# Kernel tuning notes

Hardware: AMD Instinct MI355X
Metric: run time of the kernel (lower is better)

Reference implementation:

```python
import jax, jax.numpy as jnp
import numpy as np

HEADS = 8
DIM_HEAD = 64
DIM = 512
HIDDEN = HEADS * DIM_HEAD  # 512


def setup_inputs() -> dict:
    key = jax.random.key(0)
    k1, k2, k3, k4 = jax.random.split(key, 4)
    b, m, n = 4, 8, 512
    x = jax.random.normal(k1, (b, m, n, DIM), dtype=jnp.float32)
    pos_bias = jax.random.normal(k2, (HEADS, n, 16, 16), dtype=jnp.float32)
    # torch nn.Linear(dim, 3*hidden) weight is [3*hidden, dim]; we store the
    # transposed matmul form [dim, 3*hidden] for y = x @ W.
    w_qkv = jax.random.normal(k3, (DIM, 3 * HIDDEN), dtype=jnp.float32) * (DIM ** -0.5)
    w_out = jax.random.normal(k4, (HIDDEN, DIM), dtype=jnp.float32) * (HIDDEN ** -0.5)
    return {"x": x, "pos_bias": pos_bias, "w_qkv": w_qkv, "w_out": w_out}


def reference(x, pos_bias, w_qkv, w_out):
    b, m, n, _ = x.shape
    h, d = HEADS, DIM_HEAD
    scale = d ** -0.5
    qkv = jnp.einsum('bmnc,ce->bmne', x, w_qkv)  # [b,m,n,3*hidden]
    q, k, v = jnp.split(qkv, 3, axis=-1)
    # 'b m n (h d) -> (b m) h n d'
    def to_heads(t):
        return t.reshape(b * m, n, h, d).transpose(0, 2, 1, 3)
    q, k, v = to_heads(q), to_heads(k), to_heads(v)
    q = q * scale
    sim = jnp.einsum('bhid,bhjd->bhij', q, k)  # [(b*m), h, n, n]
    # pos_bias [h, n, p, q] -> mean over last two dims -> [h, n] -> broadcast [1,h,n,1]
    pb = pos_bias.mean(axis=(-2, -1))[None, :, :, None]
    sim = sim + pb
    sim = sim - jax.lax.stop_gradient(jnp.max(sim, axis=-1, keepdims=True))
    attn = jax.nn.softmax(sim, axis=-1)
    out = jnp.einsum('bhij,bhjd->bhid', attn, v)  # [(b*m), h, n, d]
    # '(b m) h n d -> b m n (h d)'
    out = out.transpose(0, 2, 1, 3).reshape(b, m, n, h * d)
    return jnp.einsum('bmne,ec->bmnc', out, w_out)
```

## Files before the change

kernel.cpp:

```cpp
#include <hip/hip_runtime.h>
#include <stdint.h>


typedef __attribute__((ext_vector_type(8))) short bf16x8;
typedef __attribute__((ext_vector_type(4))) float f32x4;
typedef __attribute__((ext_vector_type(4))) unsigned short us4;
typedef __attribute__((ext_vector_type(4))) float float4v;

__device__ __forceinline__ unsigned short f2b(float f) {
  union { float f; uint32_t u; } x; x.f = f;
  uint32_t r = x.u + 0x7fffu + ((x.u >> 16) & 1u);
  return (unsigned short)(r >> 16);
}

__device__ __forceinline__ uint32_t cvtpk(float lo, float hi) {
  uint32_t r;
  asm("v_cvt_pk_bf16_f32 %0, %1, %2" : "=v"(r) : "v"(lo), "v"(hi));
  return r;
}

__device__ __forceinline__ f32x4 mfma16(bf16x8 a, bf16x8 b, f32x4 c) {
  return __builtin_amdgcn_mfma_f32_16x16x32_bf16(a, b, c, 0, 0, 0);
}

__device__ __forceinline__ void gload_lds16(const unsigned short* g, unsigned short* l) {
  __builtin_amdgcn_global_load_lds(
      (const __attribute__((address_space(1))) unsigned int*)g,
      (__attribute__((address_space(3))) unsigned int*)l, 16, 0, 0);
}

__global__ __launch_bounds__(256) void cast_x_kernel(
    const float* __restrict__ src, unsigned short* __restrict__ dst) {
  size_t i = ((size_t)blockIdx.x * 256 + threadIdx.x) * 4;
  float4v v = *(const float4v*)(src + i);
  us4 o;
#pragma unroll
  for (int j = 0; j < 4; ++j) o[j] = f2b(v[j]);
  *(us4*)(dst + i) = o;
}

__global__ __launch_bounds__(256) void transpose_cast_kernel(
    const float* __restrict__ src, unsigned short* __restrict__ dst, int R, int C) {
  __shared__ float tile[64][65];
  const int tc0 = blockIdx.x * 64;
  const int tr0 = blockIdx.y * 64;
#pragma unroll
  for (int k2 = 0; k2 < 16; ++k2) {
    int idx = threadIdx.x + k2 * 256;
    int r = idx >> 6, c = idx & 63;
    tile[r][c] = src[(size_t)(tr0 + r) * C + tc0 + c];
  }
  __syncthreads();
#pragma unroll
  for (int k2 = 0; k2 < 16; ++k2) {
    int idx = threadIdx.x + k2 * 256;
    int c = idx >> 6, r = idx & 63;
    dst[(size_t)(tc0 + c) * R + tr0 + r] = f2b(tile[r][c]);
  }
}

__device__ __forceinline__ void gemm_core(
    const unsigned short* __restrict__ A, const unsigned short* __restrict__ Bt,
    int K, int r0, int c0, unsigned short* As, unsigned short* Bs,
    f32x4 (&acc)[4][4]) {
  const int tid = threadIdx.x;
  const int lane = tid & 63;
  const int wave = tid >> 6;
  const int wr = (wave >> 1) * 64;
  const int wc = (wave & 1) * 64;
  const int l15 = lane & 15;
  const int g = lane >> 4;
  const int lsw = l15 & 7;

#pragma unroll
  for (int m = 0; m < 4; ++m)
#pragma unroll
    for (int n = 0; n < 4; ++n) acc[m][n] = (f32x4){0.f, 0.f, 0.f, 0.f};

  auto stage = [&](int kt, int b) {
#pragma unroll
    for (int i = 0; i < 4; ++i) {
      int chunk = tid + i * 256;
      int row = chunk >> 3;
      int csw = (chunk & 7) ^ (row & 7);
      gload_lds16(A + (size_t)(r0 + row) * K + kt + csw * 8,
                  As + b * 8192 + chunk * 8);
      gload_lds16(Bt + (size_t)(c0 + row) * K + kt + csw * 8,
                  Bs + b * 8192 + chunk * 8);
    }
  };

  stage(0, 0);
  asm volatile("s_waitcnt vmcnt(0)" ::: "memory");
  __builtin_amdgcn_s_barrier();

  const int NT = K >> 6;
  int cur = 0;
  for (int t = 0; t < NT; ++t) {
    if (t + 1 < NT) stage((t + 1) << 6, cur ^ 1);
    const unsigned short* as = As + cur * 8192;
    const unsigned short* bs = Bs + cur * 8192;
#pragma unroll
    for (int ks = 0; ks < 2; ++ks) {
      bf16x8 af[4], bfr[4];
      const int j = g + ks * 4;
      const int cj = (j ^ lsw) * 8;
#pragma unroll
      for (int m = 0; m < 4; ++m)
        af[m] = *(const bf16x8*)(as + (wr + m * 16 + l15) * 64 + cj);
#pragma unroll
      for (int n = 0; n < 4; ++n)
        bfr[n] = *(const bf16x8*)(bs + (wc + n * 16 + l15) * 64 + cj);
      __builtin_amdgcn_s_setprio(1);
#pragma unroll
      for (int m = 0; m < 4; ++m)
#pragma unroll
        for (int n = 0; n < 4; ++n) acc[m][n] = mfma16(af[m], bfr[n], acc[m][n]);
      __builtin_amdgcn_s_setprio(0);
    }
    if (t + 1 < NT) {
      asm volatile("s_waitcnt vmcnt(0)" ::: "memory");
      __builtin_amdgcn_s_barrier();
      cur ^= 1;
    }
  }
  __syncthreads();
}

__global__ __launch_bounds__(256) void gemm_qkv_kernel(
    const unsigned short* __restrict__ xb, const unsigned short* __restrict__ wqbT,
    unsigned short* __restrict__ qb, unsigned short* __restrict__ kb,
    unsigned short* __restrict__ vtb) {
  __shared__ unsigned short smem[32768];
  f32x4 acc[4][4];
  const int r0 = blockIdx.x * 128;
  const int c0 = blockIdx.y * 128;
  gemm_core(xb, wqbT, 512, r0, c0, smem, smem + 16384, acc);

  const int tid = threadIdx.x, lane = tid & 63, wave = tid >> 6;
  const int wr = (wave >> 1) * 64, wc = (wave & 1) * 64;
  const int l15 = lane & 15, g = lane >> 4;
  const int part = c0 >> 9;
  const float scl = (part == 0) ? 0.125f : 1.0f;

  if (part < 2) {
#pragma unroll
    for (int m = 0; m < 4; ++m) {
      int rbase = wr + m * 16 + 4 * g;
#pragma unroll
      for (int n = 0; n < 4; ++n) {
        int c = wc + n * 16 + l15;
        int c2 = c >> 3, ci = c & 7;
#pragma unroll
        for (int rr = 0; rr < 4; ++rr) {
          int r = rbase + rr;
          smem[r * 128 + ((c2 ^ (r & 15)) << 3) + ci] = f2b(acc[m][n][rr] * scl);
        }
      }
    }
    __syncthreads();
    unsigned short* dstb = (part == 0) ? qb : kb;
#pragma unroll
    for (int it = 0; it < 8; ++it) {
      int idx = tid + it * 256;
      int r = idx >> 4, c2 = idx & 15;
      bf16x8 v = *(const bf16x8*)(smem + r * 128 + ((c2 ^ (r & 15)) << 3));
      int e = c0 + c2 * 8;
      int rem = e & 511, h = rem >> 6, d = rem & 63;
      int ig = r0 + r;
      int bh = (ig >> 9) * 8 + h, i = ig & 511;
      *(bf16x8*)(dstb + ((size_t)bh * 512 + i) * 64 + d) = v;
    }
  } else {
#pragma unroll
    for (int m = 0; m < 4; ++m) {
      int rbase = wr + m * 16 + 4 * g;
      int r2 = rbase >> 3, rhalf = rbase & 7;
#pragma unroll
      for (int n = 0; n < 4; ++n) {
        int c = wc + n * 16 + l15;
        us4 v;
#pragma unroll
        for (int rr = 0; rr < 4; ++rr) v[rr] = f2b(acc[m][n][rr]);
        *(us4*)(smem + c * 128 + ((r2 ^ (c & 15)) << 3) + rhalf) = v;
      }
    }
    __syncthreads();
#pragma unroll
    for (int it = 0; it < 8; ++it) {
      int idx = tid + it * 256;
      int c = idx >> 4, r8 = idx & 15;
      bf16x8 v = *(const bf16x8*)(smem + c * 128 + ((r8 ^ (c & 15)) << 3));
      int e = c0 + c;
      int rem = e & 511, h = rem >> 6, d = rem & 63;
      int ig0 = r0 + r8 * 8;
      int bh = (ig0 >> 9) * 8 + h, i = ig0 & 511;
      *(bf16x8*)(vtb + ((size_t)bh * 64 + d) * 512 + i) = v;
    }
  }
}

__global__ __launch_bounds__(256) void gemm_out_kernel(
    const unsigned short* __restrict__ ao, const unsigned short* __restrict__ wobT,
    float* __restrict__ out) {
  __shared__ unsigned short smem[32768];
  f32x4 acc[4][4];
  const int r0 = blockIdx.x * 128;
  const int c0 = blockIdx.y * 128;
  gemm_core(ao, wobT, 512, r0, c0, smem, smem + 16384, acc);

  const int tid = threadIdx.x, lane = tid & 63, wave = tid >> 6;
  const int wr = (wave >> 1) * 64, wc = (wave & 1) * 64;
  const int l15 = lane & 15, g = lane >> 4;
#pragma unroll
  for (int m = 0; m < 4; ++m) {
    int i0g = r0 + wr + m * 16 + 4 * g;
#pragma unroll
    for (int n = 0; n < 4; ++n) {
      int e = c0 + wc + n * 16 + l15;
#pragma unroll
      for (int rr = 0; rr < 4; ++rr)
        out[(size_t)(i0g + rr) * 512 + e] = acc[m][n][rr];
    }
  }
}

__global__ __launch_bounds__(512, 4) void attn_kernel(
    const unsigned short* __restrict__ qb, const unsigned short* __restrict__ kb,
    const unsigned short* __restrict__ vtb, unsigned short* __restrict__ ao) {
  __shared__ unsigned short kbuf[2][8192];
  __shared__ unsigned short vbuf[2][8192];
  __shared__ unsigned short Ps[8][16][40];
  const int bh = blockIdx.x;
  const int qt = blockIdx.y;
  const int tid = threadIdx.x, lane = tid & 63, wave = tid >> 6;
  const int l15 = lane & 15, g = lane >> 4;
  const int qrow0 = qt * 128 + wave * 16;

  const unsigned short* Q = qb + ((size_t)bh * 512 + qrow0) * 64;
  const unsigned short* Kp = kb + (size_t)bh * 512 * 64;
  const unsigned short* Vt = vtb + (size_t)bh * 64 * 512;

  bf16x8 qf0 = *(const bf16x8*)(Q + l15 * 64 + g * 8);
  bf16x8 qf1 = *(const bf16x8*)(Q + l15 * 64 + 32 + g * 8);

  const int krow = tid >> 3;
  const int kck = (tid & 7) ^ (krow & 7);
  const int vrow = tid >> 4;
  const int vck = (tid & 15) ^ (vrow & 15);

  auto stage = [&](int t, int b) {
    const unsigned short* ks = Kp + ((size_t)t * 128 + krow) * 64 + kck * 8;
    gload_lds16(ks, kbuf[b] + tid * 8);
    gload_lds16(ks + 64 * 64, kbuf[b] + tid * 8 + 4096);
    const unsigned short* vs = Vt + (size_t)vrow * 512 + t * 128 + vck * 8;
    gload_lds16(vs, vbuf[b] + tid * 8);
    gload_lds16(vs + 32 * 512, vbuf[b] + tid * 8 + 4096);
  };

  f32x4 oacc[4];
#pragma unroll
  for (int m = 0; m < 4; ++m) oacc[m] = (f32x4){0.f, 0.f, 0.f, 0.f};
  float srow[4] = {0.f, 0.f, 0.f, 0.f};

  stage(0, 0);
  asm volatile("s_waitcnt vmcnt(0)" ::: "memory");
  __builtin_amdgcn_s_barrier();

  int cur = 0;
#pragma unroll
  for (int t = 0; t < 4; ++t) {
    if (t < 3) stage(t + 1, cur ^ 1);

    const unsigned short* kb_ = kbuf[cur];
    f32x4 s[8];
    const int c0i = g ^ (l15 & 7);
    __builtin_amdgcn_s_setprio(1);
#pragma unroll
    for (int tt = 0; tt < 8; ++tt) {
      int row = tt * 16 + l15;
      bf16x8 b0 = *(const bf16x8*)(kb_ + (row * 8 + c0i) * 8);
      bf16x8 b1 = *(const bf16x8*)(kb_ + (row * 8 + (c0i ^ 4)) * 8);
      f32x4 c = (f32x4){0.f, 0.f, 0.f, 0.f};
      c = mfma16(qf0, b0, c);
      s[tt] = mfma16(qf1, b1, c);
    }
    __builtin_amdgcn_s_setprio(0);

#pragma unroll
    for (int tt = 0; tt < 8; ++tt)
#pragma unroll
      for (int rr = 0; rr < 4; ++rr) {
        float e = __expf(s[tt][rr]);
        s[tt][rr] = e;
        srow[rr] += e;
      }

    const unsigned short* vb_ = vbuf[cur];
#pragma unroll
    for (int cc = 0; cc < 4; ++cc) {
#pragma unroll
      for (int rr = 0; rr < 4; ++rr) {
        uint32_t pk = cvtpk(s[cc * 2][rr], s[cc * 2 + 1][rr]);
        Ps[wave][4 * g + rr][l15] = (unsigned short)pk;
        Ps[wave][4 * g + rr][16 + l15] = (unsigned short)(pk >> 16);
      }
      asm volatile("s_waitcnt lgkmcnt(0)" ::: "memory");
      bf16x8 pf = *(const bf16x8*)(&Ps[wave][l15][g * 8]);
      __builtin_amdgcn_s_setprio(1);
#pragma unroll
      for (int m = 0; m < 4; ++m) {
        int vr = m * 16 + l15;
        bf16x8 vf = *(const bf16x8*)(vb_ + (vr * 16 + ((cc * 4 + g) ^ l15)) * 8);
        oacc[m] = mfma16(vf, pf, oacc[m]);
      }
      __builtin_amdgcn_s_setprio(0);
    }

    if (t < 3) {
      asm volatile("s_waitcnt vmcnt(0)" ::: "memory");
      __builtin_amdgcn_s_barrier();
      cur ^= 1;
    }
  }

#pragma unroll
  for (int rr = 0; rr < 4; ++rr)
#pragma unroll
    for (int o = 1; o < 16; o <<= 1) srow[rr] += __shfl_xor(srow[rr], o);
  int srcl = (l15 >> 2) * 16;
  float t0 = __shfl(srow[0], srcl), t1 = __shfl(srow[1], srcl);
  float t2 = __shfl(srow[2], srcl), t3 = __shfl(srow[3], srcl);
  int rq = l15 & 3;
  float sq = rq == 0 ? t0 : rq == 1 ? t1 : rq == 2 ? t2 : t3;
  float invq = 1.0f / sq;

  const int hh = bh & 7, bm = bh >> 3;
  unsigned short* aorow = ao + ((size_t)bm * 512 + qrow0 + l15) * 512 + hh * 64;
#pragma unroll
  for (int m = 0; m < 4; ++m) {
    union { us4 u; uint32_t w[2]; } uv;
    uv.w[0] = cvtpk(oacc[m][0] * invq, oacc[m][1] * invq);
    uv.w[1] = cvtpk(oacc[m][2] * invq, oacc[m][3] * invq);
    *(us4*)(aorow + m * 16 + 4 * g) = uv.u;
  }
}

extern "C" void kernel_launch(void* const* d_in, const int* in_sizes, int n_in,
                              void* d_out, int out_size, void* d_ws, size_t ws_size,
                              hipStream_t stream) {
  const float* x = (const float*)d_in[0];
  const float* w_qkv = (const float*)d_in[2];
  const float* w_out = (const float*)d_in[3];
  float* out = (float*)d_out;

  char* ws = (char*)d_ws;
  const size_t SZ_XB = 16384ull * 512 * 2;
  const size_t SZ_WQ = 1536ull * 512 * 2;
  const size_t SZ_WO = 512ull * 512 * 2;
  const size_t SZ_HB = 256ull * 512 * 64 * 2;
  unsigned short* xb = (unsigned short*)(ws);
  unsigned short* wqbT = (unsigned short*)(ws + SZ_XB);
  unsigned short* wobT = (unsigned short*)(ws + SZ_XB + SZ_WQ);
  unsigned short* qb = (unsigned short*)(ws + SZ_XB + SZ_WQ + SZ_WO);
  unsigned short* kb = (unsigned short*)(ws + SZ_XB + SZ_WQ + SZ_WO + SZ_HB);
  unsigned short* vtb = (unsigned short*)(ws + SZ_XB + SZ_WQ + SZ_WO + 2 * SZ_HB);
  unsigned short* ao = (unsigned short*)(ws + SZ_XB + SZ_WQ + SZ_WO + 3 * SZ_HB);

  cast_x_kernel<<<8192, 256, 0, stream>>>(x, xb);
  transpose_cast_kernel<<<dim3(1536 / 64, 512 / 64), 256, 0, stream>>>(w_qkv, wqbT, 512, 1536);
  transpose_cast_kernel<<<dim3(512 / 64, 512 / 64), 256, 0, stream>>>(w_out, wobT, 512, 512);
  gemm_qkv_kernel<<<dim3(128, 12), 256, 0, stream>>>(xb, wqbT, qb, kb, vtb);
  attn_kernel<<<dim3(256, 4), 512, 0, stream>>>(qb, kb, vtb, ao);
  gemm_out_kernel<<<dim3(128, 4), 256, 0, stream>>>(ao, wobT, out);
}
```

Baseline: 94.03 us.

## Use 256x128 GEMM tiles with 8 waves and triple-buffered LDS pipeline

Both projection GEMMs now use 512-thread blocks covering 256x128 output tiles, so each B tile is shared by twice as many rows. The K loop is fully unrolled over a fixed K=512 and uses a three-stage LDS ring with partial vmcnt waits, keeping two loads in flight while the current tile is computed. This aims to hide global load latency and cut the barrier stall after each K step. In exchange, it uses much more LDS per block (one block per CU), halves the grid size, and hardcodes K=512.

After: 99.41 us. 5.7% more time.

```diff
diff --git a/kernel.cpp b/kernel.cpp
--- a/kernel.cpp
+++ b/kernel.cpp
@@ -61,7 +61,7 @@
 
 __device__ __forceinline__ void gemm_core(
     const unsigned short* __restrict__ A, const unsigned short* __restrict__ Bt,
-    int K, int r0, int c0, unsigned short* As, unsigned short* Bs,
+    int r0, int c0, unsigned short* As, unsigned short* Bs,
     f32x4 (&acc)[4][4]) {
   const int tid = threadIdx.x;
   const int lane = tid & 63;
@@ -80,31 +80,37 @@
   auto stage = [&](int kt, int b) {
 #pragma unroll
     for (int i = 0; i < 4; ++i) {
-      int chunk = tid + i * 256;
+      int chunk = tid + i * 512;
       int row = chunk >> 3;
       int csw = (chunk & 7) ^ (row & 7);
-      gload_lds16(A + (size_t)(r0 + row) * K + kt + csw * 8,
-                  As + b * 8192 + chunk * 8);
-      gload_lds16(Bt + (size_t)(c0 + row) * K + kt + csw * 8,
+      gload_lds16(A + (size_t)(r0 + row) * 512 + kt + csw * 8,
+                  As + b * 16384 + chunk * 8);
+    }
+#pragma unroll
+    for (int i = 0; i < 2; ++i) {
+      int chunk = tid + i * 512;
+      int row = chunk >> 3;
+      int csw = (chunk & 7) ^ (row & 7);
+      gload_lds16(Bt + (size_t)(c0 + row) * 512 + kt + csw * 8,
                   Bs + b * 8192 + chunk * 8);
     }
   };
 
   stage(0, 0);
-  asm volatile("s_waitcnt vmcnt(0)" ::: "memory");
-  __builtin_amdgcn_s_barrier();
-
-  const int NT = K >> 6;
-  int cur = 0;
-  for (int t = 0; t < NT; ++t) {
-    if (t + 1 < NT) stage((t + 1) << 6, cur ^ 1);
-    const unsigned short* as = As + cur * 8192;
-    const unsigned short* bs = Bs + cur * 8192;
+  stage(64, 1);
+
+#pragma unroll
+  for (int t = 0; t < 8; ++t) {
+    if (t < 7) asm volatile("s_waitcnt vmcnt(6)" ::: "memory");
+    else       asm volatile("s_waitcnt vmcnt(0)" ::: "memory");
+    __builtin_amdgcn_s_barrier();
+    if (t < 6) stage((t + 2) * 64, (t + 2) % 3);
+    const unsigned short* as = As + (t % 3) * 16384;
+    const unsigned short* bs = Bs + (t % 3) * 8192;
 #pragma unroll
     for (int ks = 0; ks < 2; ++ks) {
       bf16x8 af[4], bfr[4];
-      const int j = g + ks * 4;
-      const int cj = (j ^ lsw) * 8;
+      const int cj = ((g + ks * 4) ^ lsw) * 8;
 #pragma unroll
       for (int m = 0; m < 4; ++m)
         af[m] = *(const bf16x8*)(as + (wr + m * 16 + l15) * 64 + cj);
@@ -118,24 +124,20 @@
         for (int n = 0; n < 4; ++n) acc[m][n] = mfma16(af[m], bfr[n], acc[m][n]);
       __builtin_amdgcn_s_setprio(0);
     }
-    if (t + 1 < NT) {
-      asm volatile("s_waitcnt vmcnt(0)" ::: "memory");
-      __builtin_amdgcn_s_barrier();
-      cur ^= 1;
-    }
   }
   __syncthreads();
 }
 
-__global__ __launch_bounds__(256) void gemm_qkv_kernel(
+__global__ __launch_bounds__(512, 1) void gemm_qkv_kernel(
     const unsigned short* __restrict__ xb, const unsigned short* __restrict__ wqbT,
     unsigned short* __restrict__ qb, unsigned short* __restrict__ kb,
     unsigned short* __restrict__ vtb) {
-  __shared__ unsigned short smem[32768];
+  __shared__ unsigned short As[49152];
+  __shared__ unsigned short Bs[24576];
   f32x4 acc[4][4];
-  const int r0 = blockIdx.x * 128;
+  const int r0 = blockIdx.x * 256;
   const int c0 = blockIdx.y * 128;
-  gemm_core(xb, wqbT, 512, r0, c0, smem, smem + 16384, acc);
+  gemm_core(xb, wqbT, r0, c0, As, Bs, acc);
 
   const int tid = threadIdx.x, lane = tid & 63, wave = tid >> 6;
   const int wr = (wave >> 1) * 64, wc = (wave & 1) * 64;
@@ -154,7 +156,7 @@
 #pragma unroll
         for (int rr = 0; rr < 4; ++rr) {
           int r = rbase + rr;
-          smem[r * 128 + ((c2 ^ (r & 15)) << 3) + ci] = f2b(acc[m][n][rr] * scl);
+          As[r * 128 + ((c2 ^ (r & 15)) << 3) + ci] = f2b(acc[m][n][rr] * scl);
         }
       }
     }
@@ -162,9 +164,9 @@
     unsigned short* dstb = (part == 0) ? qb : kb;
 #pragma unroll
     for (int it = 0; it < 8; ++it) {
-      int idx = tid + it * 256;
+      int idx = tid + it * 512;
       int r = idx >> 4, c2 = idx & 15;
-      bf16x8 v = *(const bf16x8*)(smem + r * 128 + ((c2 ^ (r & 15)) << 3));
+      bf16x8 v = *(const bf16x8*)(As + r * 128 + ((c2 ^ (r & 15)) << 3));
       int e = c0 + c2 * 8;
       int rem = e & 511, h = rem >> 6, d = rem & 63;
       int ig = r0 + r;
@@ -182,15 +184,15 @@
         us4 v;
 #pragma unroll
         for (int rr = 0; rr < 4; ++rr) v[rr] = f2b(acc[m][n][rr]);
-        *(us4*)(smem + c * 128 + ((r2 ^ (c & 15)) << 3) + rhalf) = v;
+        *(us4*)(As + c * 256 + ((r2 ^ (c & 31)) << 3) + rhalf) = v;
       }
     }
     __syncthreads();
 #pragma unroll
     for (int it = 0; it < 8; ++it) {
-      int idx = tid + it * 256;
-      int c = idx >> 4, r8 = idx & 15;
-      bf16x8 v = *(const bf16x8*)(smem + c * 128 + ((r8 ^ (c & 15)) << 3));
+      int idx = tid + it * 512;
+      int c = idx >> 5, r8 = idx & 31;
+      bf16x8 v = *(const bf16x8*)(As + c * 256 + ((r8 ^ (c & 31)) << 3));
       int e = c0 + c;
       int rem = e & 511, h = rem >> 6, d = rem & 63;
       int ig0 = r0 + r8 * 8;
@@ -200,14 +202,15 @@
   }
 }
 
-__global__ __launch_bounds__(256) void gemm_out_kernel(
+__global__ __launch_bounds__(512, 1) void gemm_out_kernel(
     const unsigned short* __restrict__ ao, const unsigned short* __restrict__ wobT,
     float* __restrict__ out) {
-  __shared__ unsigned short smem[32768];
+  __shared__ unsigned short As[49152];
+  __shared__ unsigned short Bs[24576];
   f32x4 acc[4][4];
-  const int r0 = blockIdx.x * 128;
+  const int r0 = blockIdx.x * 256;
   const int c0 = blockIdx.y * 128;
-  gemm_core(ao, wobT, 512, r0, c0, smem, smem + 16384, acc);
+  gemm_core(ao, wobT, r0, c0, As, Bs, acc);
 
   const int tid = threadIdx.x, lane = tid & 63, wave = tid >> 6;
   const int wr = (wave >> 1) * 64, wc = (wave & 1) * 64;
@@ -370,7 +373,7 @@
   cast_x_kernel<<<8192, 256, 0, stream>>>(x, xb);
   transpose_cast_kernel<<<dim3(1536 / 64, 512 / 64), 256, 0, stream>>>(w_qkv, wqbT, 512, 1536);
   transpose_cast_kernel<<<dim3(512 / 64, 512 / 64), 256, 0, stream>>>(w_out, wobT, 512, 512);
-  gemm_qkv_kernel<<<dim3(128, 12), 256, 0, stream>>>(xb, wqbT, qb, kb, vtb);
+  gemm_qkv_kernel<<<dim3(64, 12), 512, 0, stream>>>(xb, wqbT, qb, kb, vtb);
   attn_kernel<<<dim3(256, 4), 512, 0, stream>>>(qb, kb, vtb, ao);
-  gemm_out_kernel<<<dim3(128, 4), 256, 0, stream>>>(ao, wobT, out);
-}
+  gemm_out_kernel<<<dim3(64, 4), 512, 0, stream>>>(ao, wobT, out);
+}
```

## Fuse x fp32-to-bf16 cast into QKV GEMM and merge weight prep kernels

Applied to the files above, without the earlier changes.

The QKV GEMM now reads fp32 x directly through registers, converts it to bf16 with packed cvt, and writes the swizzled A tile to LDS. This removes the separate cast kernel and its 16 MB bf16 round trip. The two weight transpose-cast launches are merged into a single prep kernel, cutting launch count. In exchange, each QKV block re-reads fp32 x across its 12 column tiles (12x the fp32 traffic, mostly served from cache), uses register-staged A loads instead of direct-to-LDS loads, and adds register pressure under launch_bounds(256,2).

Result: slower. 99.91 us (+6.3%).

```diff
diff --git a/kernel.cpp b/kernel.cpp
--- a/kernel.cpp
+++ b/kernel.cpp
@@ -6,6 +6,7 @@
 typedef __attribute__((ext_vector_type(4))) float f32x4;
 typedef __attribute__((ext_vector_type(4))) unsigned short us4;
 typedef __attribute__((ext_vector_type(4))) float float4v;
+typedef __attribute__((ext_vector_type(2))) unsigned int ui2;
 
 __device__ __forceinline__ unsigned short f2b(float f) {
   union { float f; uint32_t u; } x; x.f = f;
@@ -29,21 +30,21 @@
       (__attribute__((address_space(3))) unsigned int*)l, 16, 0, 0);
 }
 
-__global__ __launch_bounds__(256) void cast_x_kernel(
-    const float* __restrict__ src, unsigned short* __restrict__ dst) {
-  size_t i = ((size_t)blockIdx.x * 256 + threadIdx.x) * 4;
-  float4v v = *(const float4v*)(src + i);
-  us4 o;
-#pragma unroll
-  for (int j = 0; j < 4; ++j) o[j] = f2b(v[j]);
-  *(us4*)(dst + i) = o;
-}
-
-__global__ __launch_bounds__(256) void transpose_cast_kernel(
-    const float* __restrict__ src, unsigned short* __restrict__ dst, int R, int C) {
+__global__ __launch_bounds__(256) void prep_kernel(
+    const float* __restrict__ wq, unsigned short* __restrict__ wqbT,
+    const float* __restrict__ wo, unsigned short* __restrict__ wobT) {
   __shared__ float tile[64][65];
-  const int tc0 = blockIdx.x * 64;
-  const int tr0 = blockIdx.y * 64;
+  const int bid = blockIdx.x;
+  const float* src;
+  unsigned short* dst;
+  int R, C, bx, by;
+  if (bid < 192) {
+    src = wq; dst = wqbT; R = 512; C = 1536; bx = bid % 24; by = bid / 24;
+  } else {
+    int q = bid - 192;
+    src = wo; dst = wobT; R = 512; C = 512; bx = q % 8; by = q / 8;
+  }
+  const int tc0 = bx * 64, tr0 = by * 64;
 #pragma unroll
   for (int k2 = 0; k2 < 16; ++k2) {
     int idx = threadIdx.x + k2 * 256;
@@ -59,52 +60,74 @@
   }
 }
 
-__device__ __forceinline__ void gemm_core(
-    const unsigned short* __restrict__ A, const unsigned short* __restrict__ Bt,
-    int K, int r0, int c0, unsigned short* As, unsigned short* Bs,
-    f32x4 (&acc)[4][4]) {
+__global__ __launch_bounds__(256, 2) void gemm_qkv_kernel(
+    const float* __restrict__ x, const unsigned short* __restrict__ wqbT,
+    unsigned short* __restrict__ qb, unsigned short* __restrict__ kb,
+    unsigned short* __restrict__ vtb) {
+  __shared__ unsigned short As[16384];
+  __shared__ unsigned short Bs[16384];
   const int tid = threadIdx.x;
-  const int lane = tid & 63;
-  const int wave = tid >> 6;
-  const int wr = (wave >> 1) * 64;
-  const int wc = (wave & 1) * 64;
-  const int l15 = lane & 15;
-  const int g = lane >> 4;
-  const int lsw = l15 & 7;
-
+  const int lane = tid & 63, wave = tid >> 6;
+  const int wr = (wave >> 1) * 64, wc = (wave & 1) * 64;
+  const int l15 = lane & 15, g = lane >> 4, lsw = l15 & 7;
+  const int r0 = blockIdx.x * 128;
+  const int c0 = blockIdx.y * 128;
+
+  f32x4 acc[4][4];
 #pragma unroll
   for (int m = 0; m < 4; ++m)
 #pragma unroll
     for (int n = 0; n < 4; ++n) acc[m][n] = (f32x4){0.f, 0.f, 0.f, 0.f};
 
-  auto stage = [&](int kt, int b) {
+  const int afc = tid & 15;
+  const int arow0 = tid >> 4;
+  float4v ar[8];
+  auto loadA = [&](int kt) {
+#pragma unroll
+    for (int i = 0; i < 8; ++i)
+      ar[i] = *(const float4v*)(x + (size_t)(r0 + arow0 + i * 16) * 512 + kt + afc * 4);
+  };
+  const int ac2 = afc >> 1, ah = afc & 1;
+  auto writeA = [&](int b) {
+#pragma unroll
+    for (int i = 0; i < 8; ++i) {
+      int row = arow0 + i * 16;
+      uint32_t w0 = cvtpk(ar[i][0], ar[i][1]);
+      uint32_t w1 = cvtpk(ar[i][2], ar[i][3]);
+      int cs = ac2 ^ (row & 7);
+      *(ui2*)(As + b * 8192 + row * 64 + cs * 8 + ah * 4) = (ui2){w0, w1};
+    }
+  };
+  auto stageB = [&](int kt, int b) {
 #pragma unroll
     for (int i = 0; i < 4; ++i) {
       int chunk = tid + i * 256;
       int row = chunk >> 3;
       int csw = (chunk & 7) ^ (row & 7);
-      gload_lds16(A + (size_t)(r0 + row) * K + kt + csw * 8,
-                  As + b * 8192 + chunk * 8);
-      gload_lds16(Bt + (size_t)(c0 + row) * K + kt + csw * 8,
+      gload_lds16(wqbT + (size_t)(c0 + row) * 512 + kt + csw * 8,
                   Bs + b * 8192 + chunk * 8);
     }
   };
 
-  stage(0, 0);
+  loadA(0);
+  stageB(0, 0);
   asm volatile("s_waitcnt vmcnt(0)" ::: "memory");
-  __builtin_amdgcn_s_barrier();
-
-  const int NT = K >> 6;
+  writeA(0);
+  __syncthreads();
+
   int cur = 0;
-  for (int t = 0; t < NT; ++t) {
-    if (t + 1 < NT) stage((t + 1) << 6, cur ^ 1);
+#pragma unroll
+  for (int t = 0; t < 8; ++t) {
+    if (t < 7) {
+      loadA((t + 1) * 64);
+      stageB((t + 1) * 64, cur ^ 1);
+    }
     const unsigned short* as = As + cur * 8192;
     const unsigned short* bs = Bs + cur * 8192;
 #pragma unroll
     for (int ks = 0; ks < 2; ++ks) {
       bf16x8 af[4], bfr[4];
-      const int j = g + ks * 4;
-      const int cj = (j ^ lsw) * 8;
+      const int cj = ((g + ks * 4) ^ lsw) * 8;
 #pragma unroll
       for (int m = 0; m < 4; ++m)
         af[m] = *(const bf16x8*)(as + (wr + m * 16 + l15) * 64 + cj);
@@ -118,28 +141,15 @@
         for (int n = 0; n < 4; ++n) acc[m][n] = mfma16(af[m], bfr[n], acc[m][n]);
       __builtin_amdgcn_s_setprio(0);
     }
-    if (t + 1 < NT) {
+    if (t < 7) {
       asm volatile("s_waitcnt vmcnt(0)" ::: "memory");
-      __builtin_amdgcn_s_barrier();
+      writeA(cur ^ 1);
+      __syncthreads();
       cur ^= 1;
     }
   }
   __syncthreads();
-}
-
-__global__ __launch_bounds__(256) void gemm_qkv_kernel(
-    const unsigned short* __restrict__ xb, const unsigned short* __restrict__ wqbT,
-    unsigned short* __restrict__ qb, unsigned short* __restrict__ kb,
-    unsigned short* __restrict__ vtb) {
-  __shared__ unsigned short smem[32768];
-  f32x4 acc[4][4];
-  const int r0 = blockIdx.x * 128;
-  const int c0 = blockIdx.y * 128;
-  gemm_core(xb, wqbT, 512, r0, c0, smem, smem + 16384, acc);
-
-  const int tid = threadIdx.x, lane = tid & 63, wave = tid >> 6;
-  const int wr = (wave >> 1) * 64, wc = (wave & 1) * 64;
-  const int l15 = lane & 15, g = lane >> 4;
+
   const int part = c0 >> 9;
   const float scl = (part == 0) ? 0.125f : 1.0f;
 
@@ -154,7 +164,7 @@
 #pragma unroll
         for (int rr = 0; rr < 4; ++rr) {
           int r = rbase + rr;
-          smem[r * 128 + ((c2 ^ (r & 15)) << 3) + ci] = f2b(acc[m][n][rr] * scl);
+          As[r * 128 + ((c2 ^ (r & 15)) << 3) + ci] = f2b(acc[m][n][rr] * scl);
         }
       }
     }
@@ -164,7 +174,7 @@
     for (int it = 0; it < 8; ++it) {
       int idx = tid + it * 256;
       int r = idx >> 4, c2 = idx & 15;
-      bf16x8 v = *(const bf16x8*)(smem + r * 128 + ((c2 ^ (r & 15)) << 3));
+      bf16x8 v = *(const bf16x8*)(As + r * 128 + ((c2 ^ (r & 15)) << 3));
       int e = c0 + c2 * 8;
       int rem = e & 511, h = rem >> 6, d = rem & 63;
       int ig = r0 + r;
@@ -182,7 +192,7 @@
         us4 v;
 #pragma unroll
         for (int rr = 0; rr < 4; ++rr) v[rr] = f2b(acc[m][n][rr]);
-        *(us4*)(smem + c * 128 + ((r2 ^ (c & 15)) << 3) + rhalf) = v;
+        *(us4*)(As + c * 128 + ((r2 ^ (c & 15)) << 3) + rhalf) = v;
       }
     }
     __syncthreads();
@@ -190,7 +200,7 @@
     for (int it = 0; it < 8; ++it) {
       int idx = tid + it * 256;
       int c = idx >> 4, r8 = idx & 15;
-      bf16x8 v = *(const bf16x8*)(smem + c * 128 + ((r8 ^ (c & 15)) << 3));
+      bf16x8 v = *(const bf16x8*)(As + c * 128 + ((r8 ^ (c & 15)) << 3));
       int e = c0 + c;
       int rem = e & 511, h = rem >> 6, d = rem & 63;
       int ig0 = r0 + r8 * 8;
@@ -203,15 +213,66 @@
 __global__ __launch_bounds__(256) void gemm_out_kernel(
     const unsigned short* __restrict__ ao, const unsigned short* __restrict__ wobT,
     float* __restrict__ out) {
-  __shared__ unsigned short smem[32768];
-  f32x4 acc[4][4];
+  __shared__ unsigned short As[16384];
+  __shared__ unsigned short Bs[16384];
+  const int tid = threadIdx.x;
+  const int lane = tid & 63, wave = tid >> 6;
+  const int wr = (wave >> 1) * 64, wc = (wave & 1) * 64;
+  const int l15 = lane & 15, g = lane >> 4, lsw = l15 & 7;
   const int r0 = blockIdx.x * 128;
   const int c0 = blockIdx.y * 128;
-  gemm_core(ao, wobT, 512, r0, c0, smem, smem + 16384, acc);
-
-  const int tid = threadIdx.x, lane = tid & 63, wave = tid >> 6;
-  const int wr = (wave >> 1) * 64, wc = (wave & 1) * 64;
-  const int l15 = lane & 15, g = lane >> 4;
+
+  f32x4 acc[4][4];
+#pragma unroll
+  for (int m = 0; m < 4; ++m)
+#pragma unroll
+    for (int n = 0; n < 4; ++n) acc[m][n] = (f32x4){0.f, 0.f, 0.f, 0.f};
+
+  auto stage = [&](int kt, int b) {
+#pragma unroll
+    for (int i = 0; i < 4; ++i) {
+      int chunk = tid + i * 256;
+      int row = chunk >> 3;
+      int csw = (chunk & 7) ^ (row & 7);
+      gload_lds16(ao + (size_t)(r0 + row) * 512 + kt + csw * 8, As + b * 8192 + chunk * 8);
+      gload_lds16(wobT + (size_t)(c0 + row) * 512 + kt + csw * 8, Bs + b * 8192 + chunk * 8);
+    }
+  };
+
+  stage(0, 0);
+  asm volatile("s_waitcnt vmcnt(0)" ::: "memory");
+  __builtin_amdgcn_s_barrier();
+
+  int cur = 0;
+#pragma unroll
+  for (int t = 0; t < 8; ++t) {
+    if (t < 7) stage((t + 1) * 64, cur ^ 1);
+    const unsigned short* as = As + cur * 8192;
+    const unsigned short* bs = Bs + cur * 8192;
+#pragma unroll
+    for (int ks = 0; ks < 2; ++ks) {
+      bf16x8 af[4], bfr[4];
+      const int cj = ((g + ks * 4) ^ lsw) * 8;
+#pragma unroll
+      for (int m = 0; m < 4; ++m)
+        af[m] = *(const bf16x8*)(as + (wr + m * 16 + l15) * 64 + cj);
+#pragma unroll
+      for (int n = 0; n < 4; ++n)
+        bfr[n] = *(const bf16x8*)(bs + (wc + n * 16 + l15) * 64 + cj);
+      __builtin_amdgcn_s_setprio(1);
+#pragma unroll
+      for (int m = 0; m < 4; ++m)
+#pragma unroll
+        for (int n = 0; n < 4; ++n) acc[m][n] = mfma16(af[m], bfr[n], acc[m][n]);
+      __builtin_amdgcn_s_setprio(0);
+    }
+    if (t < 7) {
+      asm volatile("s_waitcnt vmcnt(0)" ::: "memory");
+      __builtin_amdgcn_s_barrier();
+      cur ^= 1;
+    }
+  }
+
 #pragma unroll
   for (int m = 0; m < 4; ++m) {
     int i0g = r0 + wr + m * 16 + 4 * g;
@@ -355,22 +416,18 @@
   float* out = (float*)d_out;
 
   char* ws = (char*)d_ws;
-  const size_t SZ_XB = 16384ull * 512 * 2;
   const size_t SZ_WQ = 1536ull * 512 * 2;
   const size_t SZ_WO = 512ull * 512 * 2;
   const size_t SZ_HB = 256ull * 512 * 64 * 2;
-  unsigned short* xb = (unsigned short*)(ws);
-  unsigned short* wqbT = (unsigned short*)(ws + SZ_XB);
-  unsigned short* wobT = (unsigned short*)(ws + SZ_XB + SZ_WQ);
-  unsigned short* qb = (unsigned short*)(ws + SZ_XB + SZ_WQ + SZ_WO);
-  unsigned short* kb = (unsigned short*)(ws + SZ_XB + SZ_WQ + SZ_WO + SZ_HB);
-  unsigned short* vtb = (unsigned short*)(ws + SZ_XB + SZ_WQ + SZ_WO + 2 * SZ_HB);
-  unsigned short* ao = (unsigned short*)(ws + SZ_XB + SZ_WQ + SZ_WO + 3 * SZ_HB);
-
-  cast_x_kernel<<<8192, 256, 0, stream>>>(x, xb);
-  transpose_cast_kernel<<<dim3(1536 / 64, 512 / 64), 256, 0, stream>>>(w_qkv, wqbT, 512, 1536);
-  transpose_cast_kernel<<<dim3(512 / 64, 512 / 64), 256, 0, stream>>>(w_out, wobT, 512, 512);
-  gemm_qkv_kernel<<<dim3(128, 12), 256, 0, stream>>>(xb, wqbT, qb, kb, vtb);
+  unsigned short* wqbT = (unsigned short*)(ws);
+  unsigned short* wobT = (unsigned short*)(ws + SZ_WQ);
+  unsigned short* qb = (unsigned short*)(ws + SZ_WQ + SZ_WO);
+  unsigned short* kb = (unsigned short*)(ws + SZ_WQ + SZ_WO + SZ_HB);
+  unsigned short* vtb = (unsigned short*)(ws + SZ_WQ + SZ_WO + 2 * SZ_HB);
+  unsigned short* ao = (unsigned short*)(ws + SZ_WQ + SZ_WO + 3 * SZ_HB);
+
+  prep_kernel<<<256, 256, 0, stream>>>(w_qkv, wqbT, w_out, wobT);
+  gemm_qkv_kernel<<<dim3(128, 12), 256, 0, stream>>>(x, wqbT, qb, kb, vtb);
   attn_kernel<<<dim3(256, 4), 512, 0, stream>>>(qb, kb, vtb, ao);
   gemm_out_kernel<<<dim3(128, 4), 256, 0, stream>>>(ao, wobT, out);
 }
```
